# Kernel optimization log

Hardware: AMD Instinct MI355X
Metric: run time of the kernel (lower is better)

## Reference

```python
import jax, jax.numpy as jnp
import numpy as np

DIM = 1024
HEAD_DIM = 64
N_HEADS = DIM // HEAD_DIM  # 16
COND_DIM = 256
LENGTHS = (1, 4, 16, 64, 256, 1024)
SEQ = sum(LENGTHS)  # 1365
LN_EPS = 1e-5
ROT_D = 3 * (HEAD_DIM // 8)  # 24; 2*ROT_D = 48 <= HEAD_DIM


def _axial_pos(h, w):
    hp = np.linspace(-1.0, 1.0, h + 1); hp = (hp[:-1] + hp[1:]) / 2
    wp = np.linspace(-1.0, 1.0, w + 1); wp = (wp[:-1] + wp[1:]) / 2
    return np.stack(np.meshgrid(hp, wp, indexing='ij'), -1).reshape(h * w, 2)


def _make_theta():
    d = 5
    poses = []
    for i in range(d):
        pa = _axial_pos(32 >> i, 32 >> i)
        pr = np.full((pa.shape[0], 1), (d - i) / d)
        poses.insert(0, np.concatenate([pa, pr], -1))
    poses.insert(0, np.zeros((1, 3)))
    pos = np.concatenate(poses, 0)  # [1365, 3]
    log_min, log_max = np.log(np.pi), np.log(10 * np.pi)
    freqs = np.exp(np.linspace(log_min, log_max, HEAD_DIM // 8 * N_HEADS + 1)[:-1])
    freqs = freqs.reshape(HEAD_DIM // 8, N_HEADS).T  # [H, head_dim//8]
    th = pos[:, None, 0:1] * freqs  # [S, H, head_dim//8]
    tw = pos[:, None, 1:2] * freqs
    td = pos[:, None, 2:3] * freqs
    theta = np.concatenate([th, tw, td], -1)  # [S, H, ROT_D]
    return jnp.asarray(theta.transpose(1, 0, 2), dtype=jnp.float32)  # [H, S, ROT_D]


def _make_mask():
    m = np.zeros((SEQ, SEQ), dtype=bool)
    i = 0
    for L in LENGTHS:
        m[i:, i:i + L] = True
        i += L
    return jnp.asarray(m)


THETA = _make_theta()  # [H, S, ROT_D], constant buffer
MASK = _make_mask()    # [S, S] bool, constant buffer


def _rope(x, theta):
    # x: [B, H, S, head_dim]; theta: [H, S, ROT_D]
    d = theta.shape[-1]
    x1, x2, rest = x[..., :d], x[..., d:2 * d], x[..., 2 * d:]
    cos, sin = jnp.cos(theta), jnp.sin(theta)
    return jnp.concatenate([x1 * cos - x2 * sin, x2 * cos + x1 * sin, rest], -1)


def setup_inputs() -> dict:
    key = jax.random.key(0)
    ks = jax.random.split(key, 6)
    s = 0.02
    x = jax.random.normal(ks[0], (8, SEQ, DIM), jnp.float32)
    cond = jax.random.normal(ks[1], (8, 1, COND_DIM), jnp.float32)
    adaln_w = jax.random.normal(ks[2], (COND_DIM, 2 * DIM), jnp.float32) * s
    adaln_b = jnp.zeros((2 * DIM,), jnp.float32)
    qkv_w = jax.random.normal(ks[3], (DIM, 3 * DIM), jnp.float32) * s
    qkv_b = jnp.zeros((3 * DIM,), jnp.float32)
    out_w = jax.random.normal(ks[4], (DIM, DIM), jnp.float32) * s
    out_b = jnp.zeros((DIM,), jnp.float32)
    return {"x": x, "cond": cond, "adaln_w": adaln_w, "adaln_b": adaln_b,
            "qkv_w": qkv_w, "qkv_b": qkv_b, "out_w": out_w, "out_b": out_b}


def reference(x, cond, adaln_w, adaln_b, qkv_w, qkv_b, out_w, out_b):
    B, S, _ = x.shape
    skip = x
    # AdaLN: zero-init proj in the original; math is LN(x)*(w+1)+b
    wb = cond @ adaln_w + adaln_b  # [B, 1, 2*DIM]
    w, b = jnp.split(wb, 2, axis=-1)
    mu = x.mean(-1, keepdims=True)
    var = ((x - mu) ** 2).mean(-1, keepdims=True)
    xn = (x - mu) * jax.lax.rsqrt(var + LN_EPS)
    xn = xn * (w + 1.0) + b
    # QKV
    qkv = xn @ qkv_w + qkv_b  # [B, S, 3*DIM]
    qkv = qkv.reshape(B, S, 3, N_HEADS, HEAD_DIM).transpose(0, 3, 2, 1, 4)  # [B,H,3,S,hd]
    q, k, v = qkv[:, :, 0], qkv[:, :, 1], qkv[:, :, 2]
    theta = THETA[:, :S]  # [H, S, ROT_D]
    q = _rope(q, theta)
    k = _rope(k, theta)
    # block-causal masked SDPA
    scores = jnp.einsum('bhqd,bhkd->bhqk', q, k) / np.sqrt(HEAD_DIM).astype(np.float32)
    scores = jnp.where(MASK[:S, :S], scores, -1e30)
    attn = jax.nn.softmax(scores, axis=-1)
    o = jnp.einsum('bhqk,bhkd->bhqd', attn, v)
    o = o.transpose(0, 2, 1, 3).reshape(B, S, DIM)
    return o @ out_w + out_b + skip
```

## Files before the change

kernel.cpp:

```cpp
#include <hip/hip_runtime.h>
#include <math.h>


typedef unsigned short u16;
typedef unsigned short u16x8 __attribute__((ext_vector_type(8)));
typedef unsigned short u16x4 __attribute__((ext_vector_type(4)));
typedef __bf16        bf16x8 __attribute__((ext_vector_type(8)));
typedef float         f32x4  __attribute__((ext_vector_type(4)));

#define SEQ  1365
#define SP   1408
#define BHN  128
#define MTOT 10920
#define DIMN 1024
#define QSCALE 0.1803368801111204f

__device__ __forceinline__ u16 f2bf(float x){
  unsigned r; asm("v_cvt_pk_bf16_f32 %0, %1, %1" : "=v"(r) : "v"(x));
  return (u16)r;
}
__device__ __forceinline__ unsigned cvtpk(float a, float b){
  unsigned r; asm("v_cvt_pk_bf16_f32 %0, %1, %2" : "=v"(r) : "v"(a), "v"(b));
  return r;
}
__device__ __forceinline__ float bf2f(u16 b){
  return __builtin_bit_cast(float, ((unsigned)b) << 16);
}
__device__ __forceinline__ bf16x8 ldbf8(const u16* p){
  return __builtin_bit_cast(bf16x8, *(const u16x8*)p);
}
__device__ __forceinline__ bf16x8 ldsv(const char* p){
  return __builtin_bit_cast(bf16x8, *(const u16x8*)p);
}
__device__ __forceinline__ f32x4 mfma16(bf16x8 a, bf16x8 b, f32x4 c){
  return __builtin_amdgcn_mfma_f32_16x16x32_bf16(a, b, c, 0, 0, 0);
}
__device__ __forceinline__ void gload16(const u16* g, u16* l){
  __builtin_amdgcn_global_load_lds(
      (const __attribute__((address_space(1))) void*)(g),
      (__attribute__((address_space(3))) void*)(l), 16, 0, 0);
}

__global__ __launch_bounds__(256) void transpose_bf16(const float* __restrict__ in,
                                                      u16* __restrict__ outT,
                                                      int K, int N){
  __shared__ float tile[32][33];
  const int tx = threadIdx.x & 31, ty = threadIdx.x >> 5;
  const int n0 = blockIdx.x*32, k0 = blockIdx.y*32;
#pragma unroll
  for (int i=0;i<32;i+=8) tile[ty+i][tx] = in[(size_t)(k0+ty+i)*N + n0+tx];
  __syncthreads();
#pragma unroll
  for (int i=0;i<32;i+=8) outT[(size_t)(n0+ty+i)*K + k0+tx] = f2bf(tile[tx][ty+i]);
}

__global__ __launch_bounds__(256) void adaln_kernel(const float* __restrict__ cond,
                                                    const float* __restrict__ w,
                                                    const float* __restrict__ bsrc,
                                                    float* __restrict__ wb){
  __shared__ float cs[256];
  const int bt = blockIdx.x >> 3, ch = blockIdx.x & 7;
  const int t = threadIdx.x;
  cs[t] = cond[bt*256 + t];
  __syncthreads();
  const int n = ch*256 + t;
  float acc = bsrc[n];
  for (int j=0;j<256;j++) acc += cs[j] * w[(size_t)j*2048 + n];
  wb[bt*2048 + n] = acc;
}

__global__ __launch_bounds__(256) void theta_kernel(float* __restrict__ ctab,
                                                    float* __restrict__ stab){
  int idx = blockIdx.x*256 + threadIdx.x;
  if (idx >= 16*SEQ*24) return;
  int c = idx % 24;
  int rest = idx / 24;
  int s = rest % SEQ;
  int h = rest / SEQ;
  float p0 = 0.f, p1 = 0.f, p2 = 0.f;
  if (s >= 1){
    int start, sh; float pr;
    if      (s <   5){start=1;   sh=1; pr=0.2f;}
    else if (s <  21){start=5;   sh=2; pr=0.4f;}
    else if (s <  85){start=21;  sh=3; pr=0.6f;}
    else if (s < 341){start=85;  sh=4; pr=0.8f;}
    else             {start=341; sh=5; pr=1.0f;}
    int n = s - start;
    int row = n >> sh, colp = n & ((1<<sh)-1);
    float g = (float)(1 << sh);
    p0 = -1.f + (2*row+1)/g;
    p1 = -1.f + (2*colp+1)/g;
    p2 = pr;
  }
  int j = c & 7, comp = c >> 3;
  float kf = (float)(j*16 + h);
  float freq = 3.14159265358979323846f * exp2f(kf * (3.3219280948873623f/128.f));
  float pos = (comp==0) ? p0 : ((comp==1) ? p1 : p2);
  float th = pos * freq;
  ctab[idx] = cosf(th);
  stab[idx] = sinf(th);
}

__global__ __launch_bounds__(256) void ln_kernel(const float* __restrict__ x,
                                                 const float* __restrict__ wb,
                                                 u16* __restrict__ xn){
  const int row = blockIdx.x;
  const int b = row / SEQ;
  const int t = threadIdx.x, w = t>>6, l = t&63;
  const float4 v = ((const float4*)(x + (size_t)row*DIMN))[t];
  float s = v.x + v.y + v.z + v.w;
#pragma unroll
  for (int m=1; m<64; m<<=1) s += __shfl_xor(s, m);
  __shared__ float red1[4], red2[4];
  if (l == 0) red1[w] = s;
  __syncthreads();
  float mean = (red1[0]+red1[1]+red1[2]+red1[3]) * (1.f/1024.f);
  float dx = v.x-mean, dy = v.y-mean, dz = v.z-mean, dw = v.w-mean;
  float q = dx*dx + dy*dy + dz*dz + dw*dw;
#pragma unroll
  for (int m=1; m<64; m<<=1) q += __shfl_xor(q, m);
  if (l == 0) red2[w] = q;
  __syncthreads();
  float var = (red2[0]+red2[1]+red2[2]+red2[3]) * (1.f/1024.f);
  float rs = rsqrtf(var + 1e-5f);
  const float* wrow = wb + b*2048;
  int n0 = t*4;
  u16x4 o;
  o[0] = f2bf(dx*rs*(wrow[n0+0]+1.f) + wrow[1024+n0+0]);
  o[1] = f2bf(dy*rs*(wrow[n0+1]+1.f) + wrow[1024+n0+1]);
  o[2] = f2bf(dz*rs*(wrow[n0+2]+1.f) + wrow[1024+n0+2]);
  o[3] = f2bf(dw*rs*(wrow[n0+3]+1.f) + wrow[1024+n0+3]);
  *(u16x4*)&xn[(size_t)row*DIMN + n0] = o;
}

#define GSTAGE(dstA, dstB, koff)                                   \
  do {                                                             \
    _Pragma("unroll")                                              \
    for (int j_=0;j_<4;j_++) gload16(sA[j_]+(koff), (dstA)+j_*512);\
    _Pragma("unroll")                                              \
    for (int j_=0;j_<4;j_++) gload16(sB[j_]+(koff), (dstB)+j_*512);\
  } while(0)

__global__ __launch_bounds__(256, 2) void gemm_qkv(const u16* __restrict__ A,
                                                   const u16* __restrict__ BT,
                                                   const float* __restrict__ bias,
                                                   u16* __restrict__ qb, u16* __restrict__ kb,
                                                   u16* __restrict__ vb){
  __shared__ u16 SMEM[32768];
  u16* As0 = SMEM;        u16* As1 = SMEM + 8192;
  u16* Bs0 = SMEM + 16384; u16* Bs1 = SMEM + 24576;
  const int t = threadIdx.x, l = t & 63, w = t >> 6;
  const int lr = l & 15, lg = l >> 4;
  const int wr = w >> 1, wc = w & 1;

  const int bid = blockIdx.x;
  const int wg = (bid & 7)*264 + (bid >> 3);
  const int stile = wg/96, rr = wg - stile*96;
  const int mt = stile*4 + rr/24, nt = rr - (rr/24)*24;
  const int bat = mt / 11, mtl = mt - bat*11;
  const int s0 = mtl*128;
  const int bn = nt*128;

  const int row8 = l >> 3;
  const int gch  = (l & 7) ^ row8;
  const u16* sA[4]; const u16* sB[4];
#pragma unroll
  for (int j=0;j<4;j++){
    int srow = s0 + w*32 + j*8 + row8; if (srow > SEQ-1) srow = SEQ-1;
    sA[j] = A  + ((size_t)(bat*SEQ + srow))*1024 + gch*8;
    sB[j] = BT + (size_t)(bn + w*32 + j*8 + row8)*1024 + gch*8;
  }
  u16* dA0 = &As0[w*2048]; u16* dB0 = &Bs0[w*2048];
  u16* dA1 = &As1[w*2048]; u16* dB1 = &Bs1[w*2048];

  const int pch  = (lg ^ (lr & 7)) << 4;
  const int aoff = (wr*64 + lr)*128 + pch;
  const int boff = (wc*64 + lr)*128 + pch;

  f32x4 acc[4][4];
#pragma unroll
  for (int mi=0;mi<4;mi++)
#pragma unroll
    for (int ni=0;ni<4;ni++) acc[mi][ni] = (f32x4){0.f,0.f,0.f,0.f};

  GSTAGE(dA0, dB0, 0);
  GSTAGE(dA1, dB1, 64);
  asm volatile("s_waitcnt vmcnt(8)" ::: "memory");
  __builtin_amdgcn_s_barrier();
  __builtin_amdgcn_sched_barrier(0);

  for (int kt = 0; kt < 16; ++kt){
    const int bi = kt & 1;
    const char* Ab = (const char*)(bi ? As1 : As0);
    const char* Bb = (const char*)(bi ? Bs1 : Bs0);
    u16* dA = bi ? dA1 : dA0;
    u16* dB = bi ? dB1 : dB0;
    bf16x8 a0[4], b0[4], a1[4], b1[4];
#pragma unroll
    for (int mi=0;mi<4;mi++) a0[mi] = ldsv(Ab + (aoff + mi*2048));
#pragma unroll
    for (int ni=0;ni<4;ni++) b0[ni] = ldsv(Bb + (boff + ni*2048));
#pragma unroll
    for (int mi=0;mi<4;mi++) a1[mi] = ldsv(Ab + ((aoff + mi*2048) ^ 64));
#pragma unroll
    for (int ni=0;ni<4;ni++) b1[ni] = ldsv(Bb + ((boff + ni*2048) ^ 64));
    __builtin_amdgcn_s_setprio(1);
#pragma unroll
    for (int mi=0;mi<4;mi++)
#pragma unroll
      for (int ni=0;ni<4;ni++)
        acc[mi][ni] = mfma16(a0[mi], b0[ni], acc[mi][ni]);
    __builtin_amdgcn_s_setprio(0);
    asm volatile("s_waitcnt lgkmcnt(0)" ::: "memory");
    __builtin_amdgcn_s_barrier();
    __builtin_amdgcn_sched_barrier(0);
    if (kt < 14) GSTAGE(dA, dB, (kt+2)*64);
    __builtin_amdgcn_sched_barrier(0);
    __builtin_amdgcn_s_setprio(1);
#pragma unroll
    for (int mi=0;mi<4;mi++)
#pragma unroll
      for (int ni=0;ni<4;ni++)
        acc[mi][ni] = mfma16(a1[mi], b1[ni], acc[mi][ni]);
    __builtin_amdgcn_s_setprio(0);
    if (kt < 15){
      if (kt < 14) asm volatile("s_waitcnt vmcnt(8)" ::: "memory");
      else         asm volatile("s_waitcnt vmcnt(0)" ::: "memory");
      __builtin_amdgcn_s_barrier();
      __builtin_amdgcn_sched_barrier(0);
    }
  }

  __syncthreads();
  const int three = bn >> 10;
  const int hb = (bn & 1023) >> 6;
  if (three < 2){
    const float scl = (three==0) ? QSCALE : 1.0f;
#pragma unroll
    for (int mi=0;mi<4;mi++)
#pragma unroll
      for (int ni=0;ni<4;ni++){
        int col = wc*64 + ni*16 + lr;
        float bia = bias[bn + col];
#pragma unroll
        for (int r=0;r<4;r++){
          int ml = wr*64 + mi*16 + lg*4 + r;
          SMEM[ml*136 + col] = f2bf((acc[mi][ni][r] + bia) * scl);
        }
      }
    __syncthreads();
    u16* dst = (three==0) ? qb : kb;
    const int cs = t & 15, tm = t >> 4;
    const int h = hb + (cs>>3), d8 = (cs&7)*8;
#pragma unroll
    for (int p=0;p<8;p++){
      int ml = p*16 + tm;
      int s = s0 + ml;
      u16x8 vv = *(const u16x8*)&SMEM[ml*136 + cs*8];
      if (s < SEQ)
        *(u16x8*)&dst[((size_t)(bat*16 + h)*SP + s)*64 + d8] = vv;
    }
  } else {
#pragma unroll
    for (int mi=0;mi<4;mi++)
#pragma unroll
      for (int ni=0;ni<4;ni++){
        int col = wc*64 + ni*16 + lr;
        float bia = bias[bn + col];
#pragma unroll
        for (int r=0;r<4;r+=2){
          int ml = wr*64 + mi*16 + lg*4 + r;
          *(unsigned*)&SMEM[col*136 + ml] = cvtpk(acc[mi][ni][r]+bia, acc[mi][ni][r+1]+bia);
        }
      }
    __syncthreads();
    const int ss = t & 15, tdl = t >> 4;
    if (s0 + 127 < SEQ){
#pragma unroll
      for (int p=0;p<8;p++){
        int dl = p*16 + tdl;
        int h = hb + (dl>>6), d = dl & 63;
        u16x8 vv = *(const u16x8*)&SMEM[dl*136 + ss*8];
        *(u16x8*)&vb[((size_t)(bat*16 + h)*64 + d)*SP + s0 + ss*8] = vv;
      }
    } else {
#pragma unroll
      for (int p=0;p<8;p++){
        int dl = p*16 + tdl;
        int h = hb + (dl>>6), d = dl & 63;
        size_t rowb = ((size_t)(bat*16 + h)*64 + d)*SP;
#pragma unroll
        for (int j=0;j<8;j++){
          int s = s0 + ss*8 + j;
          if (s < SEQ) vb[rowb + s] = SMEM[dl*136 + ss*8 + j];
        }
      }
    }
  }
}

__global__ __launch_bounds__(256) void rope2_kernel(u16* __restrict__ qb,
                                                    u16* __restrict__ kb,
                                                    const float* __restrict__ ctab,
                                                    const float* __restrict__ stab){
  int rid = blockIdx.x*256 + threadIdx.x;
  if (rid >= BHN*SEQ) return;
  int bh = rid / SEQ, s = rid - bh*SEQ, h = bh & 15;
  const float* cp = ctab + (size_t)(h*SEQ + s)*24;
  const float* sp = stab + (size_t)(h*SEQ + s)*24;
  float cs[24], sn[24];
#pragma unroll
  for (int i=0;i<6;i++){
    ((float4*)cs)[i] = ((const float4*)cp)[i];
    ((float4*)sn)[i] = ((const float4*)sp)[i];
  }
  size_t base = ((size_t)bh*SP + s)*64;
  u16 buf[48];
#pragma unroll
  for (int i=0;i<6;i++) ((u16x8*)buf)[i] = *(const u16x8*)&qb[base + i*8];
#pragma unroll
  for (int j=0;j<24;j++){
    float x1 = bf2f(buf[j]), x2 = bf2f(buf[24+j]);
    buf[j]    = f2bf(x1*cs[j] - x2*sn[j]);
    buf[24+j] = f2bf(x2*cs[j] + x1*sn[j]);
  }
#pragma unroll
  for (int i=0;i<6;i++) *(u16x8*)&qb[base + i*8] = ((u16x8*)buf)[i];
#pragma unroll
  for (int i=0;i<6;i++) ((u16x8*)buf)[i] = *(const u16x8*)&kb[base + i*8];
#pragma unroll
  for (int j=0;j<24;j++){
    float x1 = bf2f(buf[j]), x2 = bf2f(buf[24+j]);
    buf[j]    = f2bf(x1*cs[j] - x2*sn[j]);
    buf[24+j] = f2bf(x2*cs[j] + x1*sn[j]);
  }
#pragma unroll
  for (int i=0;i<6;i++) *(u16x8*)&kb[base + i*8] = ((u16x8*)buf)[i];
}

__global__ __launch_bounds__(256) void attn_kernel(const u16* __restrict__ qb,
                                                   const u16* __restrict__ kb,
                                                   const u16* __restrict__ vb,
                                                   u16* __restrict__ ob){
  __shared__ u16 Ks[64*72];
  __shared__ u16 Vs[64*72];
  __shared__ u16 Ps[128*72];
  const int bx = blockIdx.x;
  const int qt = (bx < 9) ? (bx + 2) : (bx - 9);
  const int bh = blockIdx.y;
  const int t = threadIdx.x, w = t>>6, l = t&63, lr = l&15, lg = l>>4, lg4 = lg<<2;
  const u16* qB = qb + (size_t)bh*SP*64;
  const u16* kB = kb + (size_t)bh*SP*64;
  const u16* vB = vb + (size_t)bh*64*SP;
  const int q0 = qt*128 + w*32;

  bf16x8 qf[2][2];
#pragma unroll
  for (int ni=0; ni<2; ni++)
#pragma unroll
    for (int kk=0; kk<2; kk++)
      qf[ni][kk] = ldbf8(&qB[(size_t)(q0+ni*16+lr)*64 + kk*32 + lg*8]);
  const int qg0 = q0 + lr, qg1 = q0 + 16 + lr;

  f32x4 oacc[2][4];
#pragma unroll
  for (int mo=0;mo<2;mo++)
#pragma unroll
    for (int nd=0;nd<4;nd++) oacc[mo][nd] = (f32x4){0.f,0.f,0.f,0.f};
  float lst[2] = {0.f, 0.f};

  int qmax = min(qt*128+127, SEQ-1);
  int kend = (qmax<1)?1:(qmax<5)?5:(qmax<21)?21:(qmax<85)?85:(qmax<341)?341:SEQ;
  int nkt = (kend + 63) >> 6;

  for (int kt=0; kt<nkt; kt++){
    const int kbase = kt*64;
    __syncthreads();
#pragma unroll
    for (int j=0;j<2;j++){
      int flat = t + j*256;
      int row = flat >> 3, kc = (flat & 7) << 3;
      *(u16x8*)&Ks[row*72+kc] = *(const u16x8*)&kB[(size_t)(kbase+row)*64 + kc];
      *(u16x8*)&Vs[row*72+kc] = *(const u16x8*)&vB[(size_t)row*SP + kbase + kc];
    }
    __syncthreads();

    f32x4 sacc[4][2];
#pragma unroll
    for (int mi=0;mi<4;mi++){
      sacc[mi][0] = (f32x4){0.f,0.f,0.f,0.f};
      sacc[mi][1] = (f32x4){0.f,0.f,0.f,0.f};
    }
#pragma unroll
    for (int mi=0;mi<4;mi++){
      bf16x8 k0f = ldbf8(&Ks[(mi*16+lr)*72 + lg*8]);
      bf16x8 k1f = ldbf8(&Ks[(mi*16+lr)*72 + 32 + lg*8]);
      sacc[mi][0] = mfma16(k0f, qf[0][0], sacc[mi][0]);
      sacc[mi][0] = mfma16(k1f, qf[0][1], sacc[mi][0]);
      sacc[mi][1] = mfma16(k0f, qf[1][0], sacc[mi][1]);
      sacc[mi][1] = mfma16(k1f, qf[1][1], sacc[mi][1]);
    }

    int lastk = kbase + 63;
    int visLast = (lastk>=SEQ)?(1<<30):(lastk>=341)?341:(lastk>=85)?85:
                  (lastk>=21)?21:(lastk>=5)?5:(lastk>=1)?1:0;
    if (visLast > q0){
#pragma unroll
      for (int mi=0;mi<4;mi++){
        int kv = kbase + mi*16 + lg4;
#pragma unroll
        for (int r=0;r<4;r++){
          int key = kv + r;
          int visv = (key>=SEQ)?(1<<30):(key>=341)?341:(key>=85)?85:
                     (key>=21)?21:(key>=5)?5:(key>=1)?1:0;
          if (qg0 < visv) sacc[mi][0][r] = -1e30f;
          if (qg1 < visv) sacc[mi][1][r] = -1e30f;
        }
      }
    }

    float pa[2] = {0.f, 0.f}, pb[2] = {0.f, 0.f};
#pragma unroll
    for (int mi=0;mi<4;mi++)
#pragma unroll
      for (int ni=0;ni<2;ni++){
        float p0 = __builtin_amdgcn_exp2f(sacc[mi][ni][0]);
        float p1 = __builtin_amdgcn_exp2f(sacc[mi][ni][1]);
        float p2 = __builtin_amdgcn_exp2f(sacc[mi][ni][2]);
        float p3 = __builtin_amdgcn_exp2f(sacc[mi][ni][3]);
        pa[ni] += p0 + p1;
        pb[ni] += p2 + p3;
        uint2 pk = { cvtpk(p0, p1), cvtpk(p2, p3) };
        *(uint2*)&Ps[(w*32+ni*16+lr)*72 + mi*16 + lg4] = pk;
      }
#pragma unroll
    for (int ni=0;ni<2;ni++){
      float s = pa[ni] + pb[ni];
      s += __shfl_xor(s, 16);
      s += __shfl_xor(s, 32);
      lst[ni] += s;
    }

    bf16x8 pf[2][2];
#pragma unroll
    for (int mo=0;mo<2;mo++)
#pragma unroll
      for (int kk=0;kk<2;kk++)
        pf[mo][kk] = ldbf8(&Ps[(w*32+mo*16+lr)*72 + kk*32 + lg*8]);
#pragma unroll
    for (int nd=0;nd<4;nd++){
      bf16x8 v0 = ldbf8(&Vs[(nd*16+lr)*72 + lg*8]);
      bf16x8 v1 = ldbf8(&Vs[(nd*16+lr)*72 + 32 + lg*8]);
#pragma unroll
      for (int mo=0;mo<2;mo++){
        oacc[mo][nd] = mfma16(pf[mo][0], v0, oacc[mo][nd]);
        oacc[mo][nd] = mfma16(pf[mo][1], v1, oacc[mo][nd]);
      }
    }
  }

  const int b = bh >> 4, h = bh & 15;
  float linv[2][4];
#pragma unroll
  for (int mo=0;mo<2;mo++)
#pragma unroll
    for (int r=0;r<4;r++)
      linv[mo][r] = 1.f / __shfl(lst[mo], lg4 + r);
#pragma unroll
  for (int mo=0;mo<2;mo++)
#pragma unroll
    for (int r=0;r<4;r++){
      int p = q0 + mo*16 + lg4 + r;
      if (p < SEQ){
#pragma unroll
        for (int nd=0;nd<4;nd++)
          ob[((size_t)(b*SEQ + p))*DIMN + h*64 + nd*16 + lr] = f2bf(oacc[mo][nd][r] * linv[mo][r]);
      }
    }
}

__global__ __launch_bounds__(256, 2) void gemm_out(const u16* __restrict__ A,
                                                   const u16* __restrict__ BT,
                                                   const float* __restrict__ bias,
                                                   const float* __restrict__ skip,
                                                   float* __restrict__ out){
  __shared__ u16 SMEM[32768];
  u16* As0 = SMEM;        u16* As1 = SMEM + 8192;
  u16* Bs0 = SMEM + 16384; u16* Bs1 = SMEM + 24576;
  const int t = threadIdx.x, l = t & 63, w = t >> 6;
  const int lr = l & 15, lg = l >> 4;
  const int wr = w >> 1, wc = w & 1;

  const int bid = blockIdx.x;
  const int wg = (bid & 7)*88 + (bid >> 3);
  const int stile = wg/32, rr = wg & 31;
  const int mt = stile*4 + rr/8, nt = rr & 7;
  const int bat = mt / 11, mtl = mt - bat*11;
  const int s0 = mtl*128;
  const int bn = nt*128;

  const int row8 = l >> 3;
  const int gch  = (l & 7) ^ row8;
  const u16* sA[4]; const u16* sB[4];
#pragma unroll
  for (int j=0;j<4;j++){
    int srow = s0 + w*32 + j*8 + row8; if (srow > SEQ-1) srow = SEQ-1;
    sA[j] = A  + ((size_t)(bat*SEQ + srow))*1024 + gch*8;
    sB[j] = BT + (size_t)(bn + w*32 + j*8 + row8)*1024 + gch*8;
  }
  u16* dA0 = &As0[w*2048]; u16* dB0 = &Bs0[w*2048];
  u16* dA1 = &As1[w*2048]; u16* dB1 = &Bs1[w*2048];

  const int pch  = (lg ^ (lr & 7)) << 4;
  const int aoff = (wr*64 + lr)*128 + pch;
  const int boff = (wc*64 + lr)*128 + pch;

  f32x4 acc[4][4];
#pragma unroll
  for (int mi=0;mi<4;mi++)
#pragma unroll
    for (int ni=0;ni<4;ni++) acc[mi][ni] = (f32x4){0.f,0.f,0.f,0.f};

  GSTAGE(dA0, dB0, 0);
  GSTAGE(dA1, dB1, 64);
  asm volatile("s_waitcnt vmcnt(8)" ::: "memory");
  __builtin_amdgcn_s_barrier();
  __builtin_amdgcn_sched_barrier(0);

  for (int kt = 0; kt < 16; ++kt){
    const int bi = kt & 1;
    const char* Ab = (const char*)(bi ? As1 : As0);
    const char* Bb = (const char*)(bi ? Bs1 : Bs0);
    u16* dA = bi ? dA1 : dA0;
    u16* dB = bi ? dB1 : dB0;
    bf16x8 a0[4], b0[4], a1[4], b1[4];
#pragma unroll
    for (int mi=0;mi<4;mi++) a0[mi] = ldsv(Ab + (aoff + mi*2048));
#pragma unroll
    for (int ni=0;ni<4;ni++) b0[ni] = ldsv(Bb + (boff + ni*2048));
#pragma unroll
    for (int mi=0;mi<4;mi++) a1[mi] = ldsv(Ab + ((aoff + mi*2048) ^ 64));
#pragma unroll
    for (int ni=0;ni<4;ni++) b1[ni] = ldsv(Bb + ((boff + ni*2048) ^ 64));
    __builtin_amdgcn_s_setprio(1);
#pragma unroll
    for (int mi=0;mi<4;mi++)
#pragma unroll
      for (int ni=0;ni<4;ni++)
        acc[mi][ni] = mfma16(a0[mi], b0[ni], acc[mi][ni]);
    __builtin_amdgcn_s_setprio(0);
    asm volatile("s_waitcnt lgkmcnt(0)" ::: "memory");
    __builtin_amdgcn_s_barrier();
    __builtin_amdgcn_sched_barrier(0);
    if (kt < 14) GSTAGE(dA, dB, (kt+2)*64);
    __builtin_amdgcn_sched_barrier(0);
    __builtin_amdgcn_s_setprio(1);
#pragma unroll
    for (int mi=0;mi<4;mi++)
#pragma unroll
      for (int ni=0;ni<4;ni++)
        acc[mi][ni] = mfma16(a1[mi], b1[ni], acc[mi][ni]);
    __builtin_amdgcn_s_setprio(0);
    if (kt < 15){
      if (kt < 14) asm volatile("s_waitcnt vmcnt(8)" ::: "memory");
      else         asm volatile("s_waitcnt vmcnt(0)" ::: "memory");
      __builtin_amdgcn_s_barrier();
      __builtin_amdgcn_sched_barrier(0);
    }
  }

  __syncthreads();
  float* Lf = (float*)SMEM;
#pragma unroll
  for (int mi=0;mi<4;mi++)
#pragma unroll
    for (int ni=0;ni<4;ni++){
      int col = wc*64 + ni*16 + lr;
      float bia = bias[bn + col];
#pragma unroll
      for (int r=0;r<4;r++){
        int ml = wr*64 + mi*16 + lg*4 + r;
        Lf[ml*128 + col] = acc[mi][ni][r] + bia;
      }
    }
  __syncthreads();
  const int cs = t & 31, tm = t >> 5;
#pragma unroll
  for (int p=0;p<16;p++){
    int ml = p*8 + tm;
    int s = s0 + ml;
    if (s < SEQ){
      size_t idx2 = (size_t)(bat*SEQ + s)*1024 + bn + cs*4;
      float4 v4 = *(const float4*)&Lf[ml*128 + cs*4];
      const float4 sk = *(const float4*)&skip[idx2];
      float4 o4; o4.x=v4.x+sk.x; o4.y=v4.y+sk.y; o4.z=v4.z+sk.z; o4.w=v4.w+sk.w;
      *(float4*)&out[idx2] = o4;
    }
  }
}

extern "C" void kernel_launch(void* const* d_in, const int* in_sizes, int n_in,
                              void* d_out, int out_size, void* d_ws, size_t ws_size,
                              hipStream_t stream) {
  (void)in_sizes; (void)n_in; (void)out_size; (void)ws_size;
  const float* x        = (const float*)d_in[0];
  const float* cond     = (const float*)d_in[1];
  const float* adaln_w  = (const float*)d_in[2];
  const float* adaln_b  = (const float*)d_in[3];
  const float* qkv_w    = (const float*)d_in[4];
  const float* qkv_b    = (const float*)d_in[5];
  const float* out_w    = (const float*)d_in[6];
  const float* out_b    = (const float*)d_in[7];
  float* out = (float*)d_out;

  char* ws = (char*)d_ws;
  size_t off = 0;
  auto alloc = [&](size_t bytes)->void*{
    void* p = ws + off;
    off += (bytes + 255) & ~(size_t)255;
    return p;
  };
  float* wb     = (float*)alloc((size_t)8*2048*4);
  u16*   xn     = (u16*)  alloc((size_t)MTOT*DIMN*2);
  u16*   qkv_wT = (u16*)  alloc((size_t)3072*1024*2);
  u16*   out_wT = (u16*)  alloc((size_t)1024*1024*2);
  u16*   qbuf   = (u16*)  alloc((size_t)BHN*SP*64*2);
  u16*   kbuf   = (u16*)  alloc((size_t)BHN*SP*64*2);
  u16*   vbuf   = (u16*)  alloc((size_t)BHN*SP*64*2);
  float* ctab   = (float*)alloc((size_t)16*SEQ*24*4);
  float* stab   = (float*)alloc((size_t)16*SEQ*24*4);
  u16*   obuf   = xn;

  transpose_bf16<<<dim3(3072/32, 1024/32), 256, 0, stream>>>(qkv_w, qkv_wT, 1024, 3072);
  transpose_bf16<<<dim3(1024/32, 1024/32), 256, 0, stream>>>(out_w, out_wT, 1024, 1024);
  theta_kernel<<<(16*SEQ*24 + 255)/256, 256, 0, stream>>>(ctab, stab);
  adaln_kernel<<<64, 256, 0, stream>>>(cond, adaln_w, adaln_b, wb);
  ln_kernel<<<MTOT, 256, 0, stream>>>(x, wb, xn);
  gemm_qkv<<<2112, 256, 0, stream>>>(xn, qkv_wT, qkv_b, qbuf, kbuf, vbuf);
  rope2_kernel<<<(BHN*SEQ + 255)/256, 256, 0, stream>>>(qbuf, kbuf, ctab, stab);
  attn_kernel<<<dim3((SEQ+127)/128, BHN), 256, 0, stream>>>(qbuf, kbuf, vbuf, obuf);
  gemm_out<<<704, 256, 0, stream>>>(obuf, out_wT, out_b, x, out);
}
```

Measured before the change: 393.8 us.

## Double-buffer attention K/V tiles with async global-to-LDS loads and XOR swizzle

The attention kernel's synchronous K/V staging is replaced with a two-stage ring buffer filled by direct global-to-LDS loads (gload16), prefetching tile kt+2 while tile kt is consumed. The padded LDS layout is replaced with an XOR-swizzled 128-byte row layout to avoid bank conflicts, and launch bounds now request 3 blocks per CU. The aim is to hide global load latency behind the MFMA work. In exchange it uses more LDS, depends on careful vmcnt accounting (vmcnt(4) while a redundant final prefetch may be in flight), and raises register pressure.

```diff
diff --git a/kernel.cpp b/kernel.cpp
--- a/kernel.cpp
+++ b/kernel.cpp
@@ -338,12 +338,12 @@
   for (int i=0;i<6;i++) *(u16x8*)&kb[base + i*8] = ((u16x8*)buf)[i];
 }
 
-__global__ __launch_bounds__(256) void attn_kernel(const u16* __restrict__ qb,
-                                                   const u16* __restrict__ kb,
-                                                   const u16* __restrict__ vb,
-                                                   u16* __restrict__ ob){
-  __shared__ u16 Ks[64*72];
-  __shared__ u16 Vs[64*72];
+__global__ __launch_bounds__(256, 3) void attn_kernel(const u16* __restrict__ qb,
+                                                      const u16* __restrict__ kb,
+                                                      const u16* __restrict__ vb,
+                                                      u16* __restrict__ ob){
+  __shared__ u16 Ks[2][4096];
+  __shared__ u16 Vs[2][4096];
   __shared__ u16 Ps[128*72];
   const int bx = blockIdx.x;
   const int qt = (bx < 9) ? (bx + 2) : (bx - 9);
@@ -362,6 +362,26 @@
       qf[ni][kk] = ldbf8(&qB[(size_t)(q0+ni*16+lr)*64 + kk*32 + lg*8]);
   const int qg0 = q0 + lr, qg1 = q0 + 16 + lr;
 
+  const int row8 = l >> 3;
+  const int gch  = (l & 7) ^ row8;
+  const u16* sK[2]; const u16* sV[2];
+#pragma unroll
+  for (int j=0;j<2;j++){
+    sK[j] = kB + (size_t)(w*16 + j*8 + row8)*64 + gch*8;
+    sV[j] = vB + (size_t)(w*16 + j*8 + row8)*SP + gch*8;
+  }
+  const int sw0 = ((lg)   ^ (lr & 7)) << 4;
+  const int sw1 = ((4+lg) ^ (lr & 7)) << 4;
+
+#define KVSTAGE(buf_, kb_)                                          \
+  do {                                                              \
+    _Pragma("unroll")                                               \
+    for (int j_=0;j_<2;j_++){                                       \
+      gload16(sK[j_] + (kb_)*64, &Ks[buf_][(w*16+j_*8)*64]);        \
+      gload16(sV[j_] + (kb_),    &Vs[buf_][(w*16+j_*8)*64]);        \
+    }                                                               \
+  } while(0)
+
   f32x4 oacc[2][4];
 #pragma unroll
   for (int mo=0;mo<2;mo++)
@@ -373,17 +393,17 @@
   int kend = (qmax<1)?1:(qmax<5)?5:(qmax<21)?21:(qmax<85)?85:(qmax<341)?341:SEQ;
   int nkt = (kend + 63) >> 6;
 
+  KVSTAGE(0, 0);
+  KVSTAGE(1, 64);
+
   for (int kt=0; kt<nkt; kt++){
     const int kbase = kt*64;
-    __syncthreads();
-#pragma unroll
-    for (int j=0;j<2;j++){
-      int flat = t + j*256;
-      int row = flat >> 3, kc = (flat & 7) << 3;
-      *(u16x8*)&Ks[row*72+kc] = *(const u16x8*)&kB[(size_t)(kbase+row)*64 + kc];
-      *(u16x8*)&Vs[row*72+kc] = *(const u16x8*)&vB[(size_t)row*SP + kbase + kc];
-    }
-    __syncthreads();
+    const int cur = kt & 1;
+    asm volatile("s_waitcnt vmcnt(4)" ::: "memory");
+    __builtin_amdgcn_s_barrier();
+    __builtin_amdgcn_sched_barrier(0);
+    const char* Kb = (const char*)&Ks[cur][0];
+    const char* Vb = (const char*)&Vs[cur][0];
 
     f32x4 sacc[4][2];
 #pragma unroll
@@ -393,8 +413,8 @@
     }
 #pragma unroll
     for (int mi=0;mi<4;mi++){
-      bf16x8 k0f = ldbf8(&Ks[(mi*16+lr)*72 + lg*8]);
-      bf16x8 k1f = ldbf8(&Ks[(mi*16+lr)*72 + 32 + lg*8]);
+      bf16x8 k0f = ldsv(Kb + (mi*16+lr)*128 + sw0);
+      bf16x8 k1f = ldsv(Kb + (mi*16+lr)*128 + sw1);
       sacc[mi][0] = mfma16(k0f, qf[0][0], sacc[mi][0]);
       sacc[mi][0] = mfma16(k1f, qf[0][1], sacc[mi][0]);
       sacc[mi][1] = mfma16(k0f, qf[1][0], sacc[mi][1]);
@@ -449,14 +469,23 @@
         pf[mo][kk] = ldbf8(&Ps[(w*32+mo*16+lr)*72 + kk*32 + lg*8]);
 #pragma unroll
     for (int nd=0;nd<4;nd++){
-      bf16x8 v0 = ldbf8(&Vs[(nd*16+lr)*72 + lg*8]);
-      bf16x8 v1 = ldbf8(&Vs[(nd*16+lr)*72 + 32 + lg*8]);
+      bf16x8 v0 = ldsv(Vb + (nd*16+lr)*128 + sw0);
+      bf16x8 v1 = ldsv(Vb + (nd*16+lr)*128 + sw1);
 #pragma unroll
       for (int mo=0;mo<2;mo++){
         oacc[mo][nd] = mfma16(pf[mo][0], v0, oacc[mo][nd]);
         oacc[mo][nd] = mfma16(pf[mo][1], v1, oacc[mo][nd]);
       }
     }
+
+    asm volatile("s_waitcnt lgkmcnt(0)" ::: "memory");
+    __builtin_amdgcn_s_barrier();
+    __builtin_amdgcn_sched_barrier(0);
+    if (kt < nkt-1){
+      int kpf = (kt+2 < nkt ? kt+2 : nkt-1)*64;
+      KVSTAGE(cur, kpf);
+    }
+    __builtin_amdgcn_sched_barrier(0);
   }
 
   const int b = bh >> 4, h = bh & 15;
@@ -477,6 +506,7 @@
           ob[((size_t)(b*SEQ + p))*DIMN + h*64 + nd*16 + lr] = f2bf(oacc[mo][nd][r] * linv[mo][r]);
       }
     }
+#undef KVSTAGE
 }
 
 __global__ __launch_bounds__(256, 2) void gemm_out(const u16* __restrict__ A,
```

New measurement: 371.0 us. 1.06x faster.
